# Kernel tuning notes

Hardware: AMD Instinct MI355X
Metric: run time of the kernel (lower is better)

## Reference

```python
import jax, jax.numpy as jnp
import numpy as np

# EKV constants from Config
VT = 0.025
N_FACTOR = 1.5
VD = 0.5
ALPHA = 2e-06
BASE_TIA = 500000.0

KERNEL = 3
STRIDE = 1
PAD = 1


def _unfold(x, k, stride, pad):
    # torch.nn.functional.unfold: (N, C, H, W) -> (N, C*k*k, L), patch dims ordered (c, kh, kw)
    N, C, H, W = x.shape
    xp = jnp.pad(x, ((0, 0), (0, 0), (pad, pad), (pad, pad)))
    Ho = (H + 2 * pad - k) // stride + 1
    Wo = (W + 2 * pad - k) // stride + 1
    patches = []
    for i in range(k):
        for j in range(k):
            patches.append(xp[:, :, i:i + stride * Ho:stride, j:j + stride * Wo:stride])
    # (k*k, N, C, Ho, Wo) -> (N, C, k*k, Ho*Wo) -> (N, C*k*k, L)
    p = jnp.stack(patches, axis=2)  # (N, C, k*k, Ho, Wo)
    return p.reshape(N, C * k * k, Ho * Wo), Ho, Wo


def setup_inputs() -> dict:
    key = jax.random.key(0)
    k1, k2 = jax.random.split(key)
    x = jax.random.normal(k1, (4, 64, 32, 32), dtype=jnp.float32)
    # theta ~ Normal(2.5, 0.5), shape (out_channels, in_channels, k, k)
    theta = 2.5 + 0.5 * jax.random.normal(k2, (64, 64, 3, 3), dtype=jnp.float32)
    return {"x": x, "theta": theta}


def reference(x, theta):
    N, C, H, W = x.shape
    O = theta.shape[0]
    fan_in = C * KERNEL * KERNEL
    tia_gain = BASE_TIA / (fan_in ** 0.5)
    phi = 2 * N_FACTOR * VT

    x_unf, Ho, Wo = _unfold(x, KERNEL, STRIDE, PAD)      # (N, C*k*k, L)
    x_in = x_unf[:, None, :, :]                           # (N, 1, CKK, L)
    w_th = theta.reshape(1, O, -1, 1)                     # (1, O, CKK, 1)

    v_diff = x_in - w_th                                  # (N, O, CKK, L)
    f_term = jnp.square(jax.nn.softplus(v_diff / phi))
    r_term = jnp.square(jax.nn.softplus((v_diff - VD) / phi))
    i_syn = ALPHA * (f_term - r_term)
    out_current = jnp.sum(i_syn, axis=2)                  # (N, O, L)
    out_voltage = out_current * tia_gain
    return out_voltage.reshape(N, O, Ho, Wo)
```

## Files before the change

kernel.cpp:

```cpp
#include <hip/hip_runtime.h>
#include <math.h>

#define HH 32
#define WW 32
#define CIN 64
#define NO 64
#define NCK 576
#define LUT_N 1024

#define WS_W   0
#define WS_TAU 36864
#define WS_LUT 37504
#define WS_X   39552
#define X_ELEMS 262144
#define X_SLACK 8192

__global__ __launch_bounds__(256) void prep_kernel(const float* __restrict__ theta,
                                                   const float* __restrict__ x,
                                                   float* __restrict__ ws) {
    const int b = blockIdx.x, t = threadIdx.x;
    const double SZd = 19.235933878519512;
    if (b < 144) {
        int i = b * 256 + t;
        int o = i & 63, ck = i >> 6;
        ws[WS_W + i] = (float)(512.0 / (16.0 * SZd)) - theta[o * NCK + ck];
    } else if (b < 147) {
        int idx = (b - 144) * 256 + t;
        if (idx < NCK) {
            float mn = 1e30f;
            for (int o = 0; o < NO; ++o) mn = fminf(mn, theta[o * NCK + idx]);
            ws[WS_TAU + idx] = mn - 0.41588896f;
        } else if (idx < NCK + 64) {
            ws[WS_TAU + idx] = 1e30f;
        }
    } else if (b < 148) {
        const double D2 = 9.6179661929342026;
        float2* lut = (float2*)(ws + WS_LUT);
        for (int j = t; j < LUT_N; j += 256) {
            double z0 = -32.0 + j * 0.0625, z1 = z0 + 0.0625;
            double f0 = log2(1.0 + exp2(z0)), f1 = log2(1.0 + exp2(z1));
            double r0 = log2(1.0 + exp2(z0 - D2)), r1 = log2(1.0 + exp2(z1 - D2));
            double g0 = f0 * f0 - r0 * r0, g1 = f1 * f1 - r1 * r1;
            double S = g1 - g0;
            double B = g0 - S * (double)j;
            lut[j] = make_float2((float)(S * 16.0 * SZd), (float)B);
        }
    } else {
        int i = (b - 148) * 256 + t;
        ws[WS_X + i] = (i < X_ELEMS) ? x[i] : 0.0f;
    }
}

__global__ __launch_bounds__(128) void ekv_kernel(
        const float* __restrict__ ws, float* __restrict__ out) {
    constexpr float SZ16 = 307.77494205631218f;
    constexpr float OS   = 0.020018875579925058f;

    __shared__ float2 lut[LUT_N];
    __shared__ float  part[64];

    const int t = threadIdx.x;
    {
        const float2* lg = (const float2*)(ws + WS_LUT);
#pragma unroll
        for (int i = 0; i < LUT_N / 128; ++i) lut[t + 128 * i] = lg[t + 128 * i];
    }
    __syncthreads();

    const int lane = t & 63;
    const int wv   = __builtin_amdgcn_readfirstlane(t >> 6);
    const int pix  = (int)blockIdx.x;
    const int n  = pix >> 10;
    const int ho = (pix >> 5) & 31;
    const int wo = pix & 31;
    const int c0 = wv * 32;

    int l = lane;
    int c_off = l / 9; if (c_off > 6) c_off = 6;
    int k = l - 9 * c_off; if (k > 8) k = 8;
    int di = k / 3, dj = k - 3 * (k / 3);
    int h = ho + di - 1, w_ = wo + dj - 1;
    bool sval = (h >= 0) && (h < HH) && (w_ >= 0) && (w_ < WW);
    int hc = min(max(h, 0), HH - 1), wc = min(max(w_, 0), WW - 1);
    float msc = ((l < 63) && sval) ? 1.0f : 0.0f;
    int lxoff = c_off * 1024 + hc * WW + wc;

    const float* xw = ws + WS_X + (size_t)(n * CIN + c0) * 1024;
    const float* tw = ws + WS_TAU + c0 * 9;
    const float* wsW = ws + WS_W;

    float accS = 0.f, accB = 0.f;

    float xv = xw[lxoff];
    float tv = tw[l];

    for (int cb = 0; cb < 32; cb += 7) {
        int cc = 32 - cb; if (cc > 7) cc = 7;
        const float* xw2 = xw + 7 * 1024;
        const float* tw2 = tw + 7 * 9;
        float xvn = xv, tvn = tv;
        if (cb + 7 < 32) { xvn = xw2[lxoff]; tvn = tw2[l]; }

        float xs = xv * msc;
        unsigned long long act = __ballot(xs >= tv);
        act &= (1ull << (cc * 9)) - 1ull;

        if (act) {
            const int cb9 = (c0 + cb) * 9;
            int il = (int)__builtin_ctzll(act); act &= act - 1;
            float Wv = wsW[((size_t)(cb9 + il) << 6) + lane];

            while (act) {
                int il2 = (int)__builtin_ctzll(act); act &= act - 1;
                float Wv2 = wsW[((size_t)(cb9 + il2) << 6) + lane];
                int xb = __builtin_amdgcn_readlane(__builtin_bit_cast(int, xs), il);
                float sx = __builtin_bit_cast(float, xb);
                float v  = Wv + sx;
                float tf = v * SZ16;
                float tc = __builtin_amdgcn_fmed3f(tf, 0.0f, 1023.0f);
                unsigned idx = (unsigned)tc;
                float2 sb = lut[idx];
                accS = fmaf(sb.x, v, accS);
                accB += sb.y;
                il = il2; Wv = Wv2;
            }
            int xb = __builtin_amdgcn_readlane(__builtin_bit_cast(int, xs), il);
            float sx = __builtin_bit_cast(float, xb);
            float v  = Wv + sx;
            float tf = v * SZ16;
            float tc = __builtin_amdgcn_fmed3f(tf, 0.0f, 1023.0f);
            unsigned idx = (unsigned)tc;
            float2 sb = lut[idx];
            accS = fmaf(sb.x, v, accS);
            accB += sb.y;
        }
        xw = xw2; tw = tw2; xv = xvn; tv = tvn;
    }

    float p = accS + accB;
    if (wv == 1) part[lane] = p;
    __syncthreads();
    if (wv == 0)
        out[((n * NO + lane) * HH + ho) * WW + wo] = (p + part[lane]) * OS;
}

extern "C" void kernel_launch(void* const* d_in, const int* in_sizes, int n_in,
                              void* d_out, int out_size, void* d_ws, size_t ws_size,
                              hipStream_t stream) {
    const float* x     = (const float*)d_in[0];
    const float* theta = (const float*)d_in[1];
    float* out = (float*)d_out;
    float* ws  = (float*)d_ws;

    int xblocks = (X_ELEMS + X_SLACK) / 256;
    prep_kernel<<<148 + xblocks, 256, 0, stream>>>(theta, x, ws);

    ekv_kernel<<<4096, 128, 0, stream>>>(ws, out);
}
```

Baseline: 81.26 us.

## Read x directly in main kernel and unroll sparse active-entry loop by four

Drops the step that copies x into the workspace inside the prep kernel. The main kernel now reads x straight from the input with a clamped index, so the prep launch shrinks to 148 blocks. The per-wave loop over active lanes is restructured to handle four entries per iteration: four weight loads are issued up front to expose memory-level parallelism, and disabled slots are routed to LUT entry 0 so they add nothing. This costs some redundant LUT and ALU work when the active count is not a multiple of four.

```diff
diff --git a/kernel.cpp b/kernel.cpp
--- a/kernel.cpp
+++ b/kernel.cpp
@@ -7,16 +7,13 @@
 #define NO 64
 #define NCK 576
 #define LUT_N 1024
+#define X_ELEMS 262144
 
 #define WS_W   0
 #define WS_TAU 36864
 #define WS_LUT 37504
-#define WS_X   39552
-#define X_ELEMS 262144
-#define X_SLACK 8192
 
 __global__ __launch_bounds__(256) void prep_kernel(const float* __restrict__ theta,
-                                                   const float* __restrict__ x,
                                                    float* __restrict__ ws) {
     const int b = blockIdx.x, t = threadIdx.x;
     const double SZd = 19.235933878519512;
@@ -33,7 +30,7 @@
         } else if (idx < NCK + 64) {
             ws[WS_TAU + idx] = 1e30f;
         }
-    } else if (b < 148) {
+    } else {
         const double D2 = 9.6179661929342026;
         float2* lut = (float2*)(ws + WS_LUT);
         for (int j = t; j < LUT_N; j += 256) {
@@ -45,14 +42,12 @@
             double B = g0 - S * (double)j;
             lut[j] = make_float2((float)(S * 16.0 * SZd), (float)B);
         }
-    } else {
-        int i = (b - 148) * 256 + t;
-        ws[WS_X + i] = (i < X_ELEMS) ? x[i] : 0.0f;
     }
 }
 
 __global__ __launch_bounds__(128) void ekv_kernel(
-        const float* __restrict__ ws, float* __restrict__ out) {
+        const float* __restrict__ x, const float* __restrict__ ws,
+        float* __restrict__ out) {
     constexpr float SZ16 = 307.77494205631218f;
     constexpr float OS   = 0.020018875579925058f;
 
@@ -83,58 +78,63 @@
     bool sval = (h >= 0) && (h < HH) && (w_ >= 0) && (w_ < WW);
     int hc = min(max(h, 0), HH - 1), wc = min(max(w_, 0), WW - 1);
     float msc = ((l < 63) && sval) ? 1.0f : 0.0f;
-    int lxoff = c_off * 1024 + hc * WW + wc;
 
-    const float* xw = ws + WS_X + (size_t)(n * CIN + c0) * 1024;
-    const float* tw = ws + WS_TAU + c0 * 9;
+    int gidx = n * (CIN * HH * WW) + (c0 + c_off) * 1024 + hc * WW + wc;
+    const float* tw  = ws + WS_TAU + c0 * 9;
     const float* wsW = ws + WS_W;
 
     float accS = 0.f, accB = 0.f;
 
-    float xv = xw[lxoff];
+    float xv = x[min(gidx, X_ELEMS - 1)];
     float tv = tw[l];
 
     for (int cb = 0; cb < 32; cb += 7) {
         int cc = 32 - cb; if (cc > 7) cc = 7;
-        const float* xw2 = xw + 7 * 1024;
-        const float* tw2 = tw + 7 * 9;
+        int gidx2 = gidx + 7 * 1024;
+        const float* tw2 = tw + 63;
         float xvn = xv, tvn = tv;
-        if (cb + 7 < 32) { xvn = xw2[lxoff]; tvn = tw2[l]; }
+        if (cb + 7 < 32) { xvn = x[min(gidx2, X_ELEMS - 1)]; tvn = tw2[l]; }
 
         float xs = xv * msc;
         unsigned long long act = __ballot(xs >= tv);
         act &= (1ull << (cc * 9)) - 1ull;
 
-        if (act) {
-            const int cb9 = (c0 + cb) * 9;
-            int il = (int)__builtin_ctzll(act); act &= act - 1;
-            float Wv = wsW[((size_t)(cb9 + il) << 6) + lane];
+        const int cb9 = (c0 + cb) * 9;
+        while (act) {
+            unsigned long long a = act;
+            int i0 = (int)__builtin_ctzll(a);             a &= a - 1;
+            bool h1 = a != 0;
+            int i1 = a ? (int)__builtin_ctzll(a) : 0;     a &= a - 1;
+            bool h2 = a != 0;
+            int i2 = a ? (int)__builtin_ctzll(a) : 0;     a &= a - 1;
+            bool h3 = a != 0;
+            int i3 = a ? (int)__builtin_ctzll(a) : 0;     a &= a - 1;
+            act = a;
+            float W0 = wsW[((cb9 + i0) << 6) + lane];
+            float W1 = wsW[((cb9 + i1) << 6) + lane];
+            float W2 = wsW[((cb9 + i2) << 6) + lane];
+            float W3 = wsW[((cb9 + i3) << 6) + lane];
 
-            while (act) {
-                int il2 = (int)__builtin_ctzll(act); act &= act - 1;
-                float Wv2 = wsW[((size_t)(cb9 + il2) << 6) + lane];
-                int xb = __builtin_amdgcn_readlane(__builtin_bit_cast(int, xs), il);
-                float sx = __builtin_bit_cast(float, xb);
-                float v  = Wv + sx;
-                float tf = v * SZ16;
-                float tc = __builtin_amdgcn_fmed3f(tf, 0.0f, 1023.0f);
-                unsigned idx = (unsigned)tc;
-                float2 sb = lut[idx];
-                accS = fmaf(sb.x, v, accS);
-                accB += sb.y;
-                il = il2; Wv = Wv2;
+#define EKV_BODY(II, WV, EN)                                               \
+            {                                                              \
+                int xb = __builtin_amdgcn_readlane(                        \
+                             __builtin_bit_cast(int, xs), (II));           \
+                float sx = __builtin_bit_cast(float, xb);                  \
+                float v  = (WV) + sx;                                      \
+                float tf = (EN) ? v * SZ16 : -1.0f;                        \
+                float tc = __builtin_amdgcn_fmed3f(tf, 0.0f, 1023.0f);     \
+                unsigned idx = (unsigned)tc;                               \
+                float2 sb = lut[idx];                                      \
+                accS = fmaf(sb.x, v, accS);                                \
+                accB += sb.y;                                              \
             }
-            int xb = __builtin_amdgcn_readlane(__builtin_bit_cast(int, xs), il);
-            float sx = __builtin_bit_cast(float, xb);
-            float v  = Wv + sx;
-            float tf = v * SZ16;
-            float tc = __builtin_amdgcn_fmed3f(tf, 0.0f, 1023.0f);
-            unsigned idx = (unsigned)tc;
-            float2 sb = lut[idx];
-            accS = fmaf(sb.x, v, accS);
-            accB += sb.y;
+            EKV_BODY(i0, W0, true)
+            EKV_BODY(i1, W1, h1)
+            EKV_BODY(i2, W2, h2)
+            EKV_BODY(i3, W3, h3)
+#undef EKV_BODY
         }
-        xw = xw2; tw = tw2; xv = xvn; tv = tvn;
+        gidx = gidx2; tw = tw2; xv = xvn; tv = tvn;
     }
 
     float p = accS + accB;
@@ -152,8 +152,7 @@
     float* out = (float*)d_out;
     float* ws  = (float*)d_ws;
 
-    int xblocks = (X_ELEMS + X_SLACK) / 256;
-    prep_kernel<<<148 + xblocks, 256, 0, stream>>>(theta, x, ws);
+    prep_kernel<<<148, 256, 0, stream>>>(theta, ws);
 
-    ekv_kernel<<<4096, 128, 0, stream>>>(ws, out);
+    ekv_kernel<<<4096, 128, 0, stream>>>(x, ws, out);
 }
```

Result: no change. 80.17 us (-1.3%).
